# Kernel tuning notes

Hardware: AMD Instinct MI355X
Metric: run time of the kernel (lower is better)

## Reference

```python
import jax, jax.numpy as jnp
import numpy as np
import math

DIM = 768
NUM_HEADS = 12
HEAD_DIM = DIM // NUM_HEADS
ORDER = 2
SCALE = HEAD_DIM ** -0.5


def setup_inputs() -> dict:
    key = jax.random.key(0)
    ks = jax.random.split(key, 5)
    B, N, C = 8, 1024, DIM
    x = jax.random.normal(ks[0], (B, N, C), dtype=jnp.float32)
    # Linear weights stored as [in, out] so y = x @ W + b
    w_qkv = jax.random.normal(ks[1], (C, 3 * C), dtype=jnp.float32) * (C ** -0.5)
    w_proj = jax.random.normal(ks[2], (C, C), dtype=jnp.float32) * (C ** -0.5)
    b_proj = jax.random.normal(ks[3], (C,), dtype=jnp.float32) * 0.02
    return {"x": x, "w_qkv": w_qkv, "w_proj": w_proj, "b_proj": b_proj}


def reference(x, w_qkv, w_proj, b_proj):
    B, N, C = x.shape
    H, Dh = NUM_HEADS, HEAD_DIM
    qkv = (x @ w_qkv).reshape(B, N, 3, H, Dh)
    qkv = jnp.transpose(qkv, (2, 0, 3, 1, 4))  # [3, B, H, N, Dh]
    q, k, v = qkv[0], qkv[1], qkv[2]
    q = q * SCALE
    qk = jnp.einsum('bhnd,bhmd->bhnm', q, k)  # [B,H,N,N]
    # Taylor expansion: 1 + qk/1! + qk^2/2! + ... up to ORDER
    attn = jnp.ones_like(qk)
    x_power = qk
    for i in range(1, ORDER + 1):
        attn = attn + x_power / math.factorial(i)
        if i < ORDER:
            x_power = x_power * qk
    attn = jax.nn.relu(attn)
    attn = attn / jnp.sum(attn, axis=-1, keepdims=True)
    out = jnp.einsum('bhnm,bhmd->bhnd', attn, v)  # [B,H,N,Dh]
    out = jnp.transpose(out, (0, 2, 1, 3)).reshape(B, N, C)
    return out @ w_proj + b_proj
```

## Files before the change

kernel.cpp:

```cpp
#include <hip/hip_runtime.h>
#include <cstdint>

#define DIM 768
#define NHEAD 12
#define SEQ 1024
#define BATCH 8

typedef _Float16 f16x8 __attribute__((ext_vector_type(8)));
typedef __attribute__((ext_vector_type(4))) float f32x4;
typedef __attribute__((ext_vector_type(16))) float f32x16;

__device__ __forceinline__ unsigned short f2hu(float f) {
  union { _Float16 h; unsigned short u; } x;
  x.h = (_Float16)f;
  return x.u;
}
__device__ __forceinline__ unsigned int pk2(float a, float b) {
  union { _Float16 h[2]; unsigned int u; } x;
  x.h[0] = (_Float16)a;
  x.h[1] = (_Float16)b;
  return x.u;
}
__device__ __forceinline__ void gl_lds16(const void* g, void* l) {
  __builtin_amdgcn_global_load_lds(
      (const __attribute__((address_space(1))) unsigned int*)g,
      (__attribute__((address_space(3))) unsigned int*)l, 16, 0, 0);
}

__global__ __launch_bounds__(256) void prep_x(const float* __restrict__ x,
                                              unsigned short* __restrict__ a1) {
  int gid = blockIdx.x * 256 + threadIdx.x;
  int m = gid / 192;
  int c = (gid % 192) * 4;
  float4 v = *(const float4*)&x[(size_t)m * DIM + c];
  *(uint2*)&a1[(size_t)m * DIM + c] = make_uint2(pk2(v.x, v.y), pk2(v.z, v.w));
}

__global__ __launch_bounds__(256) void prep_wt(const float* __restrict__ w,
                                               unsigned short* __restrict__ wt,
                                               int N) {
  __shared__ float tile[32][33];
  int kt = blockIdx.x * 32;
  int nt = blockIdx.y * 32;
  int t = threadIdx.x;
  int c = t & 31, r8 = t >> 5;
#pragma unroll
  for (int p = 0; p < 4; ++p) {
    int k = kt + p * 8 + r8;
    tile[c][p * 8 + r8] = w[(size_t)k * N + nt + c];
  }
  __syncthreads();
#pragma unroll
  for (int p = 0; p < 4; ++p) {
    int nl = p * 8 + r8;
    wt[(size_t)(nt + nl) * DIM + kt + c] = f2hu(tile[nl][c]);
  }
}

template <int EPI>
__global__ __launch_bounds__(256) void gemm_f16(
    const unsigned short* __restrict__ A, const unsigned short* __restrict__ Bt,
    const float* __restrict__ bias, float* __restrict__ C,
    unsigned short* __restrict__ q, unsigned short* __restrict__ k,
    unsigned short* __restrict__ vt, int N) {
  __shared__ char As[16384];
  __shared__ char Bs[16384];
  const int t = threadIdx.x;
  const int l = t & 63, wv = t >> 6;
  const int g = l >> 4, l15 = l & 15;
  const int wr = wv >> 1, wc = wv & 1;
  const int m0 = blockIdx.y * 128, n0 = blockIdx.x * 128;

  f32x4 acc[4][4];
#pragma unroll
  for (int i = 0; i < 4; ++i)
#pragma unroll
    for (int j = 0; j < 4; ++j)
#pragma unroll
      for (int r = 0; r < 4; ++r) acc[i][j][r] = 0.f;

  const int rowr = t >> 3;
  const int dc = ((t & 7) ^ (rowr & 7)) * 8;

  for (int k0 = 0; k0 < DIM; k0 += 64) {
    __syncthreads();
#pragma unroll
    for (int p = 0; p < 4; ++p) {
      int row = p * 32 + rowr;
      gl_lds16(A + (size_t)(m0 + row) * DIM + k0 + dc, As + p * 4096 + wv * 1024);
      gl_lds16(Bt + (size_t)(n0 + row) * DIM + k0 + dc, Bs + p * 4096 + wv * 1024);
    }
    __syncthreads();
#pragma unroll
    for (int ks = 0; ks < 2; ++ks) {
      f16x8 af[4], bfr[4];
#pragma unroll
      for (int mf = 0; mf < 4; ++mf) {
        int row = wr * 64 + mf * 16 + l15;
        af[mf] = *(const f16x8*)(As + row * 128 + ((ks * 4 + g) ^ (row & 7)) * 16);
      }
#pragma unroll
      for (int nf = 0; nf < 4; ++nf) {
        int row = wc * 64 + nf * 16 + l15;
        bfr[nf] = *(const f16x8*)(Bs + row * 128 + ((ks * 4 + g) ^ (row & 7)) * 16);
      }
#pragma unroll
      for (int mf = 0; mf < 4; ++mf)
#pragma unroll
        for (int nf = 0; nf < 4; ++nf)
          acc[mf][nf] = __builtin_amdgcn_mfma_f32_16x16x32_f16(
              af[mf], bfr[nf], acc[mf][nf], 0, 0, 0);
    }
  }

  if (EPI == 0) {
#pragma unroll
    for (int mf = 0; mf < 4; ++mf) {
      int row = m0 + wr * 64 + mf * 16 + g * 4;
#pragma unroll
      for (int nf = 0; nf < 4; ++nf) {
        int col = n0 + wc * 64 + nf * 16 + l15;
        float bb = bias[col];
#pragma unroll
        for (int r = 0; r < 4; ++r)
          C[(size_t)(row + r) * N + col] = acc[mf][nf][r] + bb;
      }
    }
  } else {
    const int region = blockIdx.x / 6;
    const int colr0 = (blockIdx.x % 6) * 128;
#pragma unroll
    for (int mf = 0; mf < 4; ++mf) {
      int m = m0 + wr * 64 + mf * 16 + g * 4;
      int b = m >> 10, ns = m & 1023;
#pragma unroll
      for (int nf = 0; nf < 4; ++nf) {
        int colr = colr0 + wc * 64 + nf * 16 + l15;
        int hh = colr >> 6, d = colr & 63;
        size_t base = ((size_t)(b * NHEAD + hh)) << 16;
        if (region == 0) {
#pragma unroll
          for (int r = 0; r < 4; ++r)
            q[base + ((size_t)(ns + r) << 6) + d] = f2hu(acc[mf][nf][r] * 0.125f);
        } else if (region == 1) {
#pragma unroll
          for (int r = 0; r < 4; ++r)
            k[base + ((size_t)(ns + r) << 6) + d] = f2hu(acc[mf][nf][r]);
        } else {
          *(uint2*)(vt + base + ((size_t)d << 10) + ns) =
              make_uint2(pk2(acc[mf][nf][0], acc[mf][nf][1]),
                         pk2(acc[mf][nf][2], acc[mf][nf][3]));
        }
      }
    }
  }
}

__global__ __launch_bounds__(256) void attn(
    const unsigned short* __restrict__ q, const unsigned short* __restrict__ k,
    const unsigned short* __restrict__ vt, unsigned short* __restrict__ a2) {
  __shared__ char KH[8192], VT[8192];
  __shared__ float DEN[4][32];
  const int t = threadIdx.x;
  const int l = t & 63, wv = t >> 6;
  const int h = l >> 5, l31 = l & 31;
  const int bh = blockIdx.y;
  const int q0 = blockIdx.x * 128 + wv * 32;
  const size_t hb = ((size_t)bh) << 16;

  f16x8 qf[4];
#pragma unroll
  for (int ks = 0; ks < 4; ++ks)
    qf[ks] = *(const f16x8*)(q + hb + ((size_t)(q0 + l31) << 6) + ks * 16 + h * 8);

  f32x16 o0, o1;
#pragma unroll
  for (int r = 0; r < 16; ++r) { o0[r] = 0.f; o1[r] = 0.f; }
  float den = 0.f;

  const int rowr = t >> 3;
  const int dc = ((t & 7) ^ (rowr & 7)) * 8;

  for (int kt = 0; kt < 16; ++kt) {
    const int j0 = kt * 64;
    __syncthreads();
#pragma unroll
    for (int p = 0; p < 2; ++p) {
      int row = p * 32 + rowr;
      gl_lds16(k + hb + ((size_t)(j0 + row) << 6) + dc, KH + p * 4096 + wv * 1024);
      gl_lds16(vt + hb + ((size_t)row << 10) + j0 + dc, VT + p * 4096 + wv * 1024);
    }
    __syncthreads();

    f32x16 sf0, sf1;
#pragma unroll
    for (int r = 0; r < 16; ++r) { sf0[r] = 0.f; sf1[r] = 0.f; }
#pragma unroll
    for (int ks = 0; ks < 4; ++ks) {
      const int ch = ((2 * ks + h) ^ (l31 & 7)) * 16;
      sf0 = __builtin_amdgcn_mfma_f32_32x32x16_f16(
          *(const f16x8*)(KH + l31 * 128 + ch), qf[ks], sf0, 0, 0, 0);
      const int ch1 = ((2 * ks + h) ^ ((32 + l31) & 7)) * 16;
      sf1 = __builtin_amdgcn_mfma_f32_32x32x16_f16(
          *(const f16x8*)(KH + (32 + l31) * 128 + ch1), qf[ks], sf1, 0, 0, 0);
    }

    unsigned int qw[8][2];
#pragma unroll
    for (int jf = 0; jf < 2; ++jf) {
#pragma unroll
      for (int qd = 0; qd < 4; ++qd) {
        float f[4];
#pragma unroll
        for (int e = 0; e < 4; ++e) {
          float s = (jf == 0) ? sf0[qd * 4 + e] : sf1[qd * 4 + e];
          f[e] = fmaf(s, fmaf(s, 0.5f, 1.0f), 1.0f);
          den += f[e];
        }
        qw[jf * 4 + qd][0] = pk2(f[0], f[1]);
        qw[jf * 4 + qd][1] = pk2(f[2], f[3]);
      }
    }

#pragma unroll
    for (int ks = 0; ks < 4; ++ks) {
      unsigned int u00 = qw[2 * ks][0], u01 = qw[2 * ks][1];
      unsigned int u10 = qw[2 * ks + 1][0], u11 = qw[2 * ks + 1][1];
      unsigned int s00 = (unsigned)__shfl_xor((int)u00, 32, 64);
      unsigned int s01 = (unsigned)__shfl_xor((int)u01, 32, 64);
      unsigned int s10 = (unsigned)__shfl_xor((int)u10, 32, 64);
      unsigned int s11 = (unsigned)__shfl_xor((int)u11, 32, 64);
      union { unsigned int u[4]; f16x8 v; } pu;
      pu.u[0] = h ? s10 : u00;
      pu.u[1] = h ? s11 : u01;
      pu.u[2] = h ? u10 : s00;
      pu.u[3] = h ? u11 : s01;
      {
        const f16x8 vb =
            *(const f16x8*)(VT + l31 * 128 + (((2 * ks + h) ^ (l31 & 7)) * 16));
        o0 = __builtin_amdgcn_mfma_f32_32x32x16_f16(pu.v, vb, o0, 0, 0, 0);
      }
      {
        const int row = 32 + l31;
        const f16x8 vb =
            *(const f16x8*)(VT + row * 128 + (((2 * ks + h) ^ (row & 7)) * 16));
        o1 = __builtin_amdgcn_mfma_f32_32x32x16_f16(pu.v, vb, o1, 0, 0, 0);
      }
    }
  }

  den += __shfl_xor(den, 32, 64);
  if (h == 0) DEN[wv][l31] = den;
  __syncthreads();

  const int bq = (bh / NHEAD) * SEQ + q0;
  const int c0 = (bh % NHEAD) * 64;
#pragma unroll
  for (int r = 0; r < 16; ++r) {
    const int i = (r & 3) + 8 * (r >> 2) + 4 * h;
    const float inv = 1.0f / DEN[wv][i];
    const size_t row = (size_t)(bq + i) * DIM;
    a2[row + c0 + l31] = f2hu(o0[r] * inv);
    a2[row + c0 + l31 + 32] = f2hu(o1[r] * inv);
  }
}

extern "C" void kernel_launch(void* const* d_in, const int* in_sizes, int n_in,
                              void* d_out, int out_size, void* d_ws,
                              size_t ws_size, hipStream_t stream) {
  const float* x = (const float*)d_in[0];
  const float* w_qkv = (const float*)d_in[1];
  const float* w_proj = (const float*)d_in[2];
  const float* b_proj = (const float*)d_in[3];
  float* out = (float*)d_out;

  unsigned short* W1t = (unsigned short*)d_ws;
  unsigned short* W2t = W1t + (size_t)2304 * 768;
  unsigned short* A1 = W2t + (size_t)768 * 768;
  unsigned short* q = A1 + (size_t)8192 * 768;
  unsigned short* k = q + (size_t)96 * 65536;
  unsigned short* vt = k + (size_t)96 * 65536;

  const int M = BATCH * SEQ;

  prep_x<<<6144, 256, 0, stream>>>(x, A1);
  prep_wt<<<dim3(24, 72), 256, 0, stream>>>(w_qkv, W1t, 3 * DIM);
  prep_wt<<<dim3(24, 24), 256, 0, stream>>>(w_proj, W2t, DIM);

  gemm_f16<1><<<dim3(18, M / 128), 256, 0, stream>>>(A1, W1t, nullptr, nullptr,
                                                     q, k, vt, 0);

  attn<<<dim3(8, 96), 256, 0, stream>>>(q, k, vt, A1);

  gemm_f16<0><<<dim3(6, M / 128), 256, 0, stream>>>(A1, W2t, b_proj, out,
                                                    nullptr, nullptr, nullptr,
                                                    DIM);
}
```

Measured before the change: 207.3 us.

## Double-buffer K/V tiles in attention, swizzle GEMM tiles, merge weight prep

```diff
diff --git a/kernel.cpp b/kernel.cpp
--- a/kernel.cpp
+++ b/kernel.cpp
@@ -36,14 +36,23 @@
   *(uint2*)&a1[(size_t)m * DIM + c] = make_uint2(pk2(v.x, v.y), pk2(v.z, v.w));
 }
 
-__global__ __launch_bounds__(256) void prep_wt(const float* __restrict__ w,
-                                               unsigned short* __restrict__ wt,
-                                               int N) {
+__global__ __launch_bounds__(256) void prep_w(const float* __restrict__ wqkv,
+                                              const float* __restrict__ wproj,
+                                              unsigned short* __restrict__ W1t,
+                                              unsigned short* __restrict__ W2t) {
   __shared__ float tile[32][33];
-  int kt = blockIdx.x * 32;
-  int nt = blockIdx.y * 32;
-  int t = threadIdx.x;
-  int c = t & 31, r8 = t >> 5;
+  const int by = blockIdx.y;
+  const float* w;
+  unsigned short* wt;
+  int N, nt;
+  if (by < 72) {
+    w = wqkv; wt = W1t; N = 3 * DIM; nt = by * 32;
+  } else {
+    w = wproj; wt = W2t; N = DIM; nt = (by - 72) * 32;
+  }
+  const int kt = blockIdx.x * 32;
+  const int t = threadIdx.x;
+  const int c = t & 31, r8 = t >> 5;
 #pragma unroll
   for (int p = 0; p < 4; ++p) {
     int k = kt + p * 8 + r8;
@@ -69,7 +78,14 @@
   const int l = t & 63, wv = t >> 6;
   const int g = l >> 4, l15 = l & 15;
   const int wr = wv >> 1, wc = wv & 1;
-  const int m0 = blockIdx.y * 128, n0 = blockIdx.x * 128;
+
+  const int gx = (EPI == 1) ? 18 : 6;
+  const int nwg = gx * 64;
+  const int lin = blockIdx.y * gx + blockIdx.x;
+  const int cpx = nwg >> 3;
+  const int swz = (lin & 7) * cpx + (lin >> 3);
+  const int tn = swz % gx, tm = swz / gx;
+  const int m0 = tm * 128, n0 = tn * 128;
 
   f32x4 acc[4][4];
 #pragma unroll
@@ -127,8 +143,8 @@
       }
     }
   } else {
-    const int region = blockIdx.x / 6;
-    const int colr0 = (blockIdx.x % 6) * 128;
+    const int region = tn / 6;
+    const int colr0 = (tn % 6) * 128;
 #pragma unroll
     for (int mf = 0; mf < 4; ++mf) {
       int m = m0 + wr * 64 + mf * 16 + g * 4;
@@ -159,13 +175,13 @@
 __global__ __launch_bounds__(256) void attn(
     const unsigned short* __restrict__ q, const unsigned short* __restrict__ k,
     const unsigned short* __restrict__ vt, unsigned short* __restrict__ a2) {
-  __shared__ char KH[8192], VT[8192];
+  __shared__ char KH[2][8192], VT[2][8192];
   __shared__ float DEN[4][32];
   const int t = threadIdx.x;
   const int l = t & 63, wv = t >> 6;
   const int h = l >> 5, l31 = l & 31;
-  const int bh = blockIdx.y;
-  const int q0 = blockIdx.x * 128 + wv * 32;
+  const int bh = blockIdx.x;
+  const int q0 = blockIdx.y * 128 + wv * 32;
   const size_t hb = ((size_t)bh) << 16;
 
   f16x8 qf[4];
@@ -181,16 +197,23 @@
   const int rowr = t >> 3;
   const int dc = ((t & 7) ^ (rowr & 7)) * 8;
 
+#define STAGE(buf, j0)                                                        \
+  {                                                                           \
+    _Pragma("unroll") for (int p = 0; p < 2; ++p) {                           \
+      int row = p * 32 + rowr;                                                \
+      gl_lds16(k + hb + ((size_t)((j0) + row) << 6) + dc,                     \
+               KH[buf] + p * 4096 + wv * 1024);                               \
+      gl_lds16(vt + hb + ((size_t)row << 10) + (j0) + dc,                     \
+               VT[buf] + p * 4096 + wv * 1024);                               \
+    }                                                                         \
+  }
+
+  STAGE(0, 0);
+  __syncthreads();
+
+  int buf = 0;
   for (int kt = 0; kt < 16; ++kt) {
-    const int j0 = kt * 64;
-    __syncthreads();
-#pragma unroll
-    for (int p = 0; p < 2; ++p) {
-      int row = p * 32 + rowr;
-      gl_lds16(k + hb + ((size_t)(j0 + row) << 6) + dc, KH + p * 4096 + wv * 1024);
-      gl_lds16(vt + hb + ((size_t)row << 10) + j0 + dc, VT + p * 4096 + wv * 1024);
-    }
-    __syncthreads();
+    if (kt < 15) STAGE(buf ^ 1, (kt + 1) * 64);
 
     f32x16 sf0, sf1;
 #pragma unroll
@@ -199,10 +222,9 @@
     for (int ks = 0; ks < 4; ++ks) {
       const int ch = ((2 * ks + h) ^ (l31 & 7)) * 16;
       sf0 = __builtin_amdgcn_mfma_f32_32x32x16_f16(
-          *(const f16x8*)(KH + l31 * 128 + ch), qf[ks], sf0, 0, 0, 0);
-      const int ch1 = ((2 * ks + h) ^ ((32 + l31) & 7)) * 16;
+          *(const f16x8*)(KH[buf] + l31 * 128 + ch), qf[ks], sf0, 0, 0, 0);
       sf1 = __builtin_amdgcn_mfma_f32_32x32x16_f16(
-          *(const f16x8*)(KH + (32 + l31) * 128 + ch1), qf[ks], sf1, 0, 0, 0);
+          *(const f16x8*)(KH[buf] + (32 + l31) * 128 + ch), qf[ks], sf1, 0, 0, 0);
     }
 
     unsigned int qw[8][2];
@@ -235,23 +257,19 @@
       pu.u[1] = h ? s11 : u01;
       pu.u[2] = h ? u10 : s00;
       pu.u[3] = h ? u11 : s01;
-      {
-        const f16x8 vb =
-            *(const f16x8*)(VT + l31 * 128 + (((2 * ks + h) ^ (l31 & 7)) * 16));
-        o0 = __builtin_amdgcn_mfma_f32_32x32x16_f16(pu.v, vb, o0, 0, 0, 0);
-      }
-      {
-        const int row = 32 + l31;
-        const f16x8 vb =
-            *(const f16x8*)(VT + row * 128 + (((2 * ks + h) ^ (row & 7)) * 16));
-        o1 = __builtin_amdgcn_mfma_f32_32x32x16_f16(pu.v, vb, o1, 0, 0, 0);
-      }
-    }
+      const int ch = ((2 * ks + h) ^ (l31 & 7)) * 16;
+      o0 = __builtin_amdgcn_mfma_f32_32x32x16_f16(
+          pu.v, *(const f16x8*)(VT[buf] + l31 * 128 + ch), o0, 0, 0, 0);
+      o1 = __builtin_amdgcn_mfma_f32_32x32x16_f16(
+          pu.v, *(const f16x8*)(VT[buf] + (32 + l31) * 128 + ch), o1, 0, 0, 0);
+    }
+
+    __syncthreads();
+    buf ^= 1;
   }
 
   den += __shfl_xor(den, 32, 64);
   if (h == 0) DEN[wv][l31] = den;
-  __syncthreads();
 
   const int bq = (bh / NHEAD) * SEQ + q0;
   const int c0 = (bh % NHEAD) * 64;
@@ -284,13 +302,12 @@
   const int M = BATCH * SEQ;
 
   prep_x<<<6144, 256, 0, stream>>>(x, A1);
-  prep_wt<<<dim3(24, 72), 256, 0, stream>>>(w_qkv, W1t, 3 * DIM);
-  prep_wt<<<dim3(24, 24), 256, 0, stream>>>(w_proj, W2t, DIM);
+  prep_w<<<dim3(24, 96), 256, 0, stream>>>(w_qkv, w_proj, W1t, W2t);
 
   gemm_f16<1><<<dim3(18, M / 128), 256, 0, stream>>>(A1, W1t, nullptr, nullptr,
                                                      q, k, vt, 0);
 
-  attn<<<dim3(8, 96), 256, 0, stream>>>(q, k, vt, A1);
+  attn<<<dim3(96, 8), 256, 0, stream>>>(q, k, vt, A1);
 
   gemm_f16<0><<<dim3(6, M / 128), 256, 0, stream>>>(A1, W2t, b_proj, out,
                                                     nullptr, nullptr, nullptr,
```

New measurement: 206.3 us. Within noise of the previous version (-0.5%).
